# Kernel tuning notes

Hardware: AMD Instinct MI355X
Metric: run time of the kernel (lower is better)

Reference implementation:

```python
import jax, jax.numpy as jnp
import numpy as np

B, N, C, H, V = 32, 1024, 512, 256, 50  # batch, positions, post_conv_out_channels, hidden_size, out_channels


def setup_inputs() -> dict:
    key = jax.random.key(0)
    ks = jax.random.split(key, 9)
    s = 0.05
    p = lambda k, shape: jax.random.normal(k, shape, jnp.float32) * s
    return dict(
        features=jax.random.normal(ks[0], (B, N, C), jnp.float32),
        w_i2h=p(ks[1], (H, C)),              # input_to_hidden (no bias)
        w_h2h=p(ks[2], (H, H)), b_h2h=jnp.zeros((H,), jnp.float32),
        w_score=p(ks[3], (H,)),              # score Linear(H,1,no bias)
        w_gru_ih=p(ks[4], (3 * H, C + V)), w_gru_hh=p(ks[5], (3 * H, H)),
        b_gru_ih=jnp.zeros((3 * H,), jnp.float32), b_gru_hh=jnp.zeros((3 * H,), jnp.float32),
        w_s1=p(ks[6], (H, H)), b_s1=jnp.zeros((H,), jnp.float32),
        w_s2=p(ks[7], (V, H)), b_s2=jnp.zeros((V,), jnp.float32),
        max_text_length=500,
    )


def reference(features, w_i2h, w_h2h, b_h2h, w_score, w_gru_ih, w_gru_hh,
              b_gru_ih, b_gru_hh, w_s1, b_s1, w_s2, b_s2, max_text_length):
    batch = features.shape[0]
    hid = w_h2h.shape[0]
    vocab = w_s2.shape[0]
    steps = max_text_length + 1
    # input_to_hidden(features) is loop-invariant -> hoist out of the recurrence
    feat_proj = jnp.einsum('bnc,hc->bnh', features, w_i2h)

    def gru_cell(x, h):
        gi = x @ w_gru_ih.T + b_gru_ih
        gh = h @ w_gru_hh.T + b_gru_hh
        i_r, i_z, i_n = jnp.split(gi, 3, axis=-1)
        h_r, h_z, h_n = jnp.split(gh, 3, axis=-1)
        r = jax.nn.sigmoid(i_r + h_r)
        z = jax.nn.sigmoid(i_z + h_z)
        n = jnp.tanh(i_n + r * h_n)
        return (1.0 - z) * n + z * h

    def step(carry, _):
        h, pre = carry
        prev_proj = h @ w_h2h.T + b_h2h                      # [B,H]
        scores = jnp.tanh(feat_proj + prev_proj[:, None, :]) @ w_score  # [B,N]
        alpha = jax.nn.softmax(scores, axis=1)
        ctx = jnp.einsum('bn,bnc->bc', alpha, features)      # [B,C]
        onehot = jax.nn.one_hot(pre, vocab, dtype=features.dtype)
        h_new = gru_cell(jnp.concatenate([ctx, onehot], axis=-1), h)
        struct = (h_new @ w_s1.T + b_s1) @ w_s2.T + b_s2     # structure_generator, [B,V]
        pre_new = jnp.argmax(struct, axis=-1)
        return (h_new, pre_new), struct

    h0 = jnp.zeros((batch, hid), features.dtype)
    pre0 = jnp.zeros((batch,), jnp.int32)
    _, structs = jax.lax.scan(step, (h0, pre0), None, length=steps)  # [T,B,V]
    structs = jnp.transpose(structs, (1, 0, 2))                      # [B,T,V]
    return jax.nn.softmax(structs, axis=-1)
```

## Files before the change

kernel.cpp:

```cpp
#include <hip/hip_runtime.h>
#include <math.h>

#define B_ 32
#define N_ 1024
#define C_ 512
#define H_ 256
#define V_ 50
#define T_ 501
#define CV_ 562
#define G3_ 768
#define CHUNKS_ 32
#define POSB_ 32

typedef float    f32x4 __attribute__((ext_vector_type(4)));
typedef _Float16 f16x4 __attribute__((ext_vector_type(4)));
typedef _Float16 f16x8 __attribute__((ext_vector_type(8)));

__device__ __forceinline__ float fast_rcp(float x) { return __builtin_amdgcn_rcpf(x); }
__device__ __forceinline__ float fast_tanh(float x) {
  float e = __expf(2.0f * x);
  return 1.0f - 2.0f * fast_rcp(e + 1.0f);
}
__device__ __forceinline__ float fast_sigmoid(float x) {
  return fast_rcp(1.0f + __expf(-x));
}

__global__ __launch_bounds__(256) void fp_gemm(const float* __restrict__ A,
                                               const float* __restrict__ W,
                                               _Float16* __restrict__ FPh) {
  __shared__ __align__(16) float As[16][68];
  __shared__ __align__(16) float Ws[16][68];
  const int t = threadIdx.x;
  const int m0 = blockIdx.x * 64;
  const int h0 = blockIdx.y * 64;
  const int lr = t & 63;
  const int kg = t >> 6;
  const int tx = t & 15, ty = t >> 4;
  float acc[4][4] = {};
  for (int k0 = 0; k0 < C_; k0 += 16) {
    float4 av = *(const float4*)&A[(size_t)(m0 + lr) * C_ + k0 + kg * 4];
    float4 wv = *(const float4*)&W[(size_t)(h0 + lr) * C_ + k0 + kg * 4];
    As[kg*4+0][lr] = av.x; As[kg*4+1][lr] = av.y; As[kg*4+2][lr] = av.z; As[kg*4+3][lr] = av.w;
    Ws[kg*4+0][lr] = wv.x; Ws[kg*4+1][lr] = wv.y; Ws[kg*4+2][lr] = wv.z; Ws[kg*4+3][lr] = wv.w;
    __syncthreads();
#pragma unroll
    for (int kk = 0; kk < 16; ++kk) {
      float4 a = *(const float4*)&As[kk][ty * 4];
      float4 w = *(const float4*)&Ws[kk][tx * 4];
      acc[0][0] += a.x*w.x; acc[0][1] += a.x*w.y; acc[0][2] += a.x*w.z; acc[0][3] += a.x*w.w;
      acc[1][0] += a.y*w.x; acc[1][1] += a.y*w.y; acc[1][2] += a.y*w.z; acc[1][3] += a.y*w.w;
      acc[2][0] += a.z*w.x; acc[2][1] += a.z*w.y; acc[2][2] += a.z*w.z; acc[2][3] += a.z*w.w;
      acc[3][0] += a.w*w.x; acc[3][1] += a.w*w.y; acc[3][2] += a.w*w.z; acc[3][3] += a.w*w.w;
    }
    __syncthreads();
  }
#pragma unroll
  for (int i = 0; i < 4; ++i) {
    f16x4 o;
    o.x = (_Float16)acc[i][0]; o.y = (_Float16)acc[i][1];
    o.z = (_Float16)acc[i][2]; o.w = (_Float16)acc[i][3];
    *(f16x4*)&FPh[(size_t)(m0 + ty*4 + i) * H_ + h0 + tx*4] = o;
  }
}

__global__ void feat_to_fp16(const float* __restrict__ src, _Float16* __restrict__ dst,
                             int total4) {
  int i = blockIdx.x * 256 + threadIdx.x;
  if (i >= total4) return;
  f32x4 v = *(const f32x4*)&src[(size_t)i * 4];
  f16x4 o; o.x = (_Float16)v.x; o.y = (_Float16)v.y; o.z = (_Float16)v.z; o.w = (_Float16)v.w;
  *(f16x4*)&dst[(size_t)i * 4] = o;
}

__global__ void transpose_split(const float* __restrict__ src, float* __restrict__ dstA,
                                float* __restrict__ dstB, int rows, int cols, int splitc) {
  int i = blockIdx.x * 256 + threadIdx.x;
  if (i >= rows * cols) return;
  int j = i / cols, c = i - j * cols;
  float v = src[i];
  if (c < splitc) dstA[(size_t)c * rows + j] = v;
  else            dstB[(size_t)(c - splitc) * rows + j] = v;
}

__global__ void init_kernel(const float* __restrict__ b_h2h, float* __restrict__ h,
                            float* __restrict__ pp, int* __restrict__ pre) {
  int i = blockIdx.x * blockDim.x + threadIdx.x;
  if (i < B_ * H_) { h[i] = 0.0f; pp[i] = b_h2h[i & (H_ - 1)]; }
  if (i < B_) pre[i] = 0;
}

__global__ __launch_bounds__(256) void k1_attn(
    const _Float16* __restrict__ feath, const _Float16* __restrict__ fph,
    const float* __restrict__ w_score, const float* __restrict__ pp,
    float* __restrict__ part_ctx, float* __restrict__ part_l) {
  __shared__ __align__(16) float lds_ctx[4 * C_];
  __shared__ float lds_l[4];

  const int t = threadIdx.x;
  const int wv = t >> 6;
  const int lane = t & 63;
  const int b = blockIdx.x >> 5;
  const int chunk = blockIdx.x & (CHUNKS_ - 1);

  float4 ppr = *(const float4*)&pp[b * H_ + lane * 4];
  float4 wsr = *(const float4*)&w_score[lane * 4];
  float aA0 = 0.f, aA1 = 0.f, aA2 = 0.f, aA3 = 0.f;
  float aB0 = 0.f, aB1 = 0.f, aB2 = 0.f, aB3 = 0.f;
  float lacc = 0.f;
  const _Float16* fphb = fph + (size_t)b * N_ * H_;
  const _Float16* fbb  = feath + (size_t)b * N_ * C_;
  const int n0 = chunk * POSB_ + wv * 8;
#pragma unroll 2
  for (int i = 0; i < 8; ++i) {
    const int n = n0 + i;
    f16x4 v = __builtin_nontemporal_load((const f16x4*)&fphb[(size_t)n * H_ + lane * 4]);
    float s = fast_tanh((float)v.x + ppr.x) * wsr.x + fast_tanh((float)v.y + ppr.y) * wsr.y
            + fast_tanh((float)v.z + ppr.z) * wsr.z + fast_tanh((float)v.w + ppr.w) * wsr.w;
#pragma unroll
    for (int off = 32; off > 0; off >>= 1) s += __shfl_xor(s, off);
    float p = __expf(s);
    lacc += p;
    f16x8 f = __builtin_nontemporal_load((const f16x8*)&fbb[(size_t)n * C_ + lane * 8]);
    aA0 += p * (float)f.s0; aA1 += p * (float)f.s1; aA2 += p * (float)f.s2; aA3 += p * (float)f.s3;
    aB0 += p * (float)f.s4; aB1 += p * (float)f.s5; aB2 += p * (float)f.s6; aB3 += p * (float)f.s7;
  }
  {
    float4 o0; o0.x = aA0; o0.y = aA1; o0.z = aA2; o0.w = aA3;
    float4 o1; o1.x = aB0; o1.y = aB1; o1.z = aB2; o1.w = aB3;
    *(float4*)&lds_ctx[wv * C_ + lane * 8] = o0;
    *(float4*)&lds_ctx[wv * C_ + lane * 8 + 4] = o1;
  }
  if (lane == 0) lds_l[wv] = lacc;
  __syncthreads();
  {
    float c0 = lds_ctx[t] + lds_ctx[C_ + t] + lds_ctx[2 * C_ + t] + lds_ctx[3 * C_ + t];
    float c1 = lds_ctx[t + 256] + lds_ctx[C_ + t + 256] + lds_ctx[2 * C_ + t + 256] + lds_ctx[3 * C_ + t + 256];
    float* pc = &part_ctx[((size_t)b * CHUNKS_ + chunk) * C_];
    pc[t] = c0;
    pc[t + 256] = c1;
    if (t == 0) part_l[b * CHUNKS_ + chunk] = lds_l[0] + lds_l[1] + lds_l[2] + lds_l[3];
  }
}

__global__ __launch_bounds__(512) void kred(
    const float* __restrict__ part_ctx, const float* __restrict__ part_l,
    float* __restrict__ ctx_raw, float* __restrict__ l_total) {
  const int b = blockIdx.x;
  const int t = threadIdx.x;
  const float* src = part_ctx + (size_t)b * CHUNKS_ * C_ + t;
  float s = 0.f;
#pragma unroll 8
  for (int ch = 0; ch < CHUNKS_; ++ch) s += src[(size_t)ch * C_];
  ctx_raw[b * C_ + t] = s;
  if (t < 64) {
    float lv = (t < CHUNKS_) ? part_l[b * CHUNKS_ + t] : 0.0f;
#pragma unroll
    for (int off = 32; off > 0; off >>= 1) lv += __shfl_xor(lv, off);
    if (t == 0) l_total[b] = lv;
  }
}

__global__ __launch_bounds__(256) void k2a_gates(
    const float* __restrict__ ctx_raw, const float* __restrict__ h,
    const float* __restrict__ WtA, const float* __restrict__ WtH,
    float* __restrict__ pgi, float* __restrict__ pgh) {
  __shared__ __align__(16) float wlds[64][64];
  __shared__ __align__(16) float clds[32][64];
  const int t = threadIdx.x;
  const int j0 = blockIdx.x * 64;
  const int ks = blockIdx.y;
  const int jl = (t & 31) * 2;
  const int b0 = (t >> 5) * 4;

  float acc[2][4] = {};
#pragma unroll
  for (int kt = 0; kt < 2; ++kt) {
    const int k0 = ks * 128 + kt * 64;
    __syncthreads();
#pragma unroll
    for (int q = 0; q < 4; ++q) {
      int idx = q * 256 + t; int r = idx >> 4, f4 = (idx & 15) * 4;
      *(float4*)&wlds[r][f4] = *(const float4*)&WtA[(size_t)(k0 + r) * G3_ + j0 + f4];
    }
#pragma unroll
    for (int q = 0; q < 2; ++q) {
      int idx = q * 256 + t; int bb = idx >> 4, f4 = (idx & 15) * 4;
      *(float4*)&clds[bb][f4] = *(const float4*)&ctx_raw[(size_t)bb * C_ + k0 + f4];
    }
    __syncthreads();
#pragma unroll 8
    for (int k = 0; k < 64; ++k) {
      float w0 = wlds[k][jl], w1 = wlds[k][jl + 1];
      float x0 = clds[b0][k], x1 = clds[b0 + 1][k], x2 = clds[b0 + 2][k], x3 = clds[b0 + 3][k];
      acc[0][0] += w0 * x0; acc[0][1] += w0 * x1; acc[0][2] += w0 * x2; acc[0][3] += w0 * x3;
      acc[1][0] += w1 * x0; acc[1][1] += w1 * x1; acc[1][2] += w1 * x2; acc[1][3] += w1 * x3;
    }
  }
#pragma unroll
  for (int i = 0; i < 2; ++i)
#pragma unroll
    for (int q = 0; q < 4; ++q)
      pgi[((size_t)ks * B_ + b0 + q) * G3_ + j0 + jl + i] = acc[i][q];

  float acb[2][4] = {};
  {
    const int k0 = ks * 64;
    __syncthreads();
#pragma unroll
    for (int q = 0; q < 4; ++q) {
      int idx = q * 256 + t; int r = idx >> 4, f4 = (idx & 15) * 4;
      *(float4*)&wlds[r][f4] = *(const float4*)&WtH[(size_t)(k0 + r) * G3_ + j0 + f4];
    }
#pragma unroll
    for (int q = 0; q < 2; ++q) {
      int idx = q * 256 + t; int bb = idx >> 4, f4 = (idx & 15) * 4;
      *(float4*)&clds[bb][f4] = *(const float4*)&h[(size_t)bb * H_ + k0 + f4];
    }
    __syncthreads();
#pragma unroll 8
    for (int k = 0; k < 64; ++k) {
      float w0 = wlds[k][jl], w1 = wlds[k][jl + 1];
      float x0 = clds[b0][k], x1 = clds[b0 + 1][k], x2 = clds[b0 + 2][k], x3 = clds[b0 + 3][k];
      acb[0][0] += w0 * x0; acb[0][1] += w0 * x1; acb[0][2] += w0 * x2; acb[0][3] += w0 * x3;
      acb[1][0] += w1 * x0; acb[1][1] += w1 * x1; acb[1][2] += w1 * x2; acb[1][3] += w1 * x3;
    }
  }
#pragma unroll
  for (int i = 0; i < 2; ++i)
#pragma unroll
    for (int q = 0; q < 4; ++q)
      pgh[((size_t)ks * B_ + b0 + q) * G3_ + j0 + jl + i] = acb[i][q];
}

__global__ __launch_bounds__(512) void k2b_tail(
    int tstep,
    const float* __restrict__ pgi, const float* __restrict__ pgh,
    const float* __restrict__ l_total,
    const float* __restrict__ WtO,
    const float* __restrict__ b_gru_ih, const float* __restrict__ b_gru_hh,
    const float* __restrict__ Wt_s1, const float* __restrict__ b_s1,
    const float* __restrict__ Wt_h2h, const float* __restrict__ b_h2h,
    const float* __restrict__ w_s2, const float* __restrict__ b_s2,
    float* __restrict__ h, float* __restrict__ pp, int* __restrict__ pre,
    float* __restrict__ out) {
  __shared__ __align__(16) float shn[H_];
  __shared__ __align__(16) float ss1[H_];
  __shared__ float sst[64];
  const int b = blockIdx.x;
  const int t = threadIdx.x;
  const int prev = pre[b];
  const float invl = 1.0f / l_total[b];

  if (t < H_) {
    float gi0 = 0.f, gi1 = 0.f, gi2 = 0.f, gh0 = 0.f, gh1 = 0.f, gh2 = 0.f;
#pragma unroll
    for (int ks = 0; ks < 4; ++ks) {
      const float* pg = pgi + ((size_t)ks * B_ + b) * G3_;
      const float* ph = pgh + ((size_t)ks * B_ + b) * G3_;
      gi0 += pg[t]; gi1 += pg[t + 256]; gi2 += pg[t + 512];
      gh0 += ph[t]; gh1 += ph[t + 256]; gh2 += ph[t + 512];
    }
    const float* wo = WtO + (size_t)prev * G3_;
    gi0 = gi0 * invl + b_gru_ih[t]       + wo[t];
    gi1 = gi1 * invl + b_gru_ih[t + 256] + wo[t + 256];
    gi2 = gi2 * invl + b_gru_ih[t + 512] + wo[t + 512];
    gh0 += b_gru_hh[t]; gh1 += b_gru_hh[t + 256]; gh2 += b_gru_hh[t + 512];
    const float h_old = h[b * H_ + t];
    const float r = fast_sigmoid(gi0 + gh0);
    const float z = fast_sigmoid(gi1 + gh1);
    const float nn = fast_tanh(gi2 + r * gh2);
    const float hnew = (1.0f - z) * nn + z * h_old;
    h[b * H_ + t] = hnew;
    shn[t] = hnew;
  }
  __syncthreads();

  if (t < H_) {
    float acc = b_s1[t];
    const float* w1 = Wt_s1 + t;
#pragma unroll 8
    for (int c = 0; c < H_; ++c) acc += w1[(size_t)c * H_] * shn[c];
    ss1[t] = acc;
  } else if (t < 2 * H_) {
    const int tt = t - H_;
    float acc = b_h2h[tt];
    const float* wh2 = Wt_h2h + tt;
#pragma unroll 8
    for (int c = 0; c < H_; ++c) acc += wh2[(size_t)c * H_] * shn[c];
    pp[b * H_ + tt] = acc;
  }
  __syncthreads();

  const int wv = t >> 6, lane = t & 63;
  for (int v = wv; v < V_; v += 8) {
    float4 wr = *(const float4*)&w_s2[(size_t)v * H_ + lane * 4];
    float4 sv = *(const float4*)&ss1[lane * 4];
    float acc = wr.x * sv.x + wr.y * sv.y + wr.z * sv.z + wr.w * sv.w;
#pragma unroll
    for (int off = 32; off > 0; off >>= 1) acc += __shfl_xor(acc, off);
    if (lane == 0) sst[v] = acc + b_s2[v];
  }
  __syncthreads();

  if (t < 64) {
    float val = (lane < V_) ? sst[lane] : -INFINITY;
    float m = val;
#pragma unroll
    for (int off = 32; off > 0; off >>= 1) m = fmaxf(m, __shfl_xor(m, off));
    unsigned long long msk = __ballot(val == m);
    int amax = __ffsll(msk) - 1;
    float e = (lane < V_) ? __expf(val - m) : 0.0f;
    float ssum = e;
#pragma unroll
    for (int off = 32; off > 0; off >>= 1) ssum += __shfl_xor(ssum, off);
    if (lane < V_) out[((size_t)b * T_ + tstep) * V_ + lane] = e / ssum;
    if (lane == 0) pre[b] = amax;
  }
}

extern "C" void kernel_launch(void* const* d_in, const int* in_sizes, int n_in,
                              void* d_out, int out_size, void* d_ws, size_t ws_size,
                              hipStream_t stream) {
  (void)in_sizes; (void)n_in; (void)out_size; (void)ws_size;
  const float* feat     = (const float*)d_in[0];
  const float* w_i2h    = (const float*)d_in[1];
  const float* w_h2h    = (const float*)d_in[2];
  const float* b_h2h    = (const float*)d_in[3];
  const float* w_score  = (const float*)d_in[4];
  const float* w_gru_ih = (const float*)d_in[5];
  const float* w_gru_hh = (const float*)d_in[6];
  const float* b_gru_ih = (const float*)d_in[7];
  const float* b_gru_hh = (const float*)d_in[8];
  const float* w_s1     = (const float*)d_in[9];
  const float* b_s1     = (const float*)d_in[10];
  const float* w_s2     = (const float*)d_in[11];
  const float* b_s2     = (const float*)d_in[12];
  float* out = (float*)d_out;

  char* ws = (char*)d_ws;
  size_t off = 0;
  auto alloc = [&](size_t bytes) { void* p = ws + off; off += (bytes + 255) & ~(size_t)255; return p; };
  _Float16* fph   = (_Float16*)alloc((size_t)B_ * N_ * H_ * 2);
  _Float16* feath = (_Float16*)alloc((size_t)B_ * N_ * C_ * 2);
  float* part_ctx = (float*)alloc((size_t)B_ * CHUNKS_ * C_ * 4);
  float* part_l   = (float*)alloc((size_t)B_ * CHUNKS_ * 4);
  float* ctx_raw  = (float*)alloc((size_t)B_ * C_ * 4);
  float* l_total  = (float*)alloc((size_t)B_ * 4);
  float* pgi      = (float*)alloc((size_t)4 * B_ * G3_ * 4);
  float* pgh      = (float*)alloc((size_t)4 * B_ * G3_ * 4);
  float* WtA      = (float*)alloc((size_t)C_ * G3_ * 4);
  float* WtO      = (float*)alloc((size_t)V_ * G3_ * 4);
  float* WtH      = (float*)alloc((size_t)H_ * G3_ * 4);
  float* Wt_s1    = (float*)alloc((size_t)H_ * H_ * 4);
  float* Wt_h2h   = (float*)alloc((size_t)H_ * H_ * 4);
  float* h        = (float*)alloc((size_t)B_ * H_ * 4);
  float* pp       = (float*)alloc((size_t)B_ * H_ * 4);
  int*   pre      = (int*)alloc((size_t)B_ * 4);

  init_kernel<<<32, 256, 0, stream>>>(b_h2h, h, pp, pre);
  fp_gemm<<<dim3((B_ * N_) / 64, H_ / 64), 256, 0, stream>>>(feat, w_i2h, fph);
  feat_to_fp16<<<(B_ * N_ * C_ / 4 + 255) / 256, 256, 0, stream>>>(feat, feath, B_ * N_ * C_ / 4);
  transpose_split<<<(G3_ * CV_ + 255) / 256, 256, 0, stream>>>(w_gru_ih, WtA, WtO, G3_, CV_, C_);
  transpose_split<<<(G3_ * H_ + 255) / 256, 256, 0, stream>>>(w_gru_hh, WtH, WtH, G3_, H_, H_);
  transpose_split<<<(H_ * H_ + 255) / 256, 256, 0, stream>>>(w_s1, Wt_s1, Wt_s1, H_, H_, H_);
  transpose_split<<<(H_ * H_ + 255) / 256, 256, 0, stream>>>(w_h2h, Wt_h2h, Wt_h2h, H_, H_, H_);

  for (int tstep = 0; tstep < T_; ++tstep) {
    k1_attn<<<B_ * CHUNKS_, 256, 0, stream>>>(feath, fph, w_score, pp, part_ctx, part_l);
    kred<<<B_, 512, 0, stream>>>(part_ctx, part_l, ctx_raw, l_total);
    k2a_gates<<<dim3(12, 4), 256, 0, stream>>>(ctx_raw, h, WtA, WtH, pgi, pgh);
    k2b_tail<<<B_, 512, 0, stream>>>(tstep, pgi, pgh, l_total, WtO,
                                     b_gru_ih, b_gru_hh, Wt_s1, b_s1, Wt_h2h, b_h2h,
                                     w_s2, b_s2, h, pp, pre, out);
  }
}
```

Measured before the change: 15.99 ms.

## Fuse per-step reduction and GRU tail into fewer kernels with atomic last-block handoff

Drops the separate reduction kernel: the last attention block per batch element, chosen by an atomic ticket counter, sums the partial contexts. The gate GEMM and GRU tail are merged into one 48-block kernel. The first 16 blocks to finish exit, and the remaining 32 spin until all 48 have published their gate partials, then each runs the GRU update and output head for one batch element. This cuts per-step kernel launches from four to two. The cost is atomic counters, relaxed atomic loads and stores, and a spin-wait that assumes all 48 blocks are co-resident.

```diff
diff --git a/kernel.cpp b/kernel.cpp
--- a/kernel.cpp
+++ b/kernel.cpp
@@ -23,6 +23,15 @@
 }
 __device__ __forceinline__ float fast_sigmoid(float x) {
   return fast_rcp(1.0f + __expf(-x));
+}
+__device__ __forceinline__ void astore(float* p, float v) {
+  __hip_atomic_store(p, v, __ATOMIC_RELAXED, __HIP_MEMORY_SCOPE_AGENT);
+}
+__device__ __forceinline__ float aload(const float* p) {
+  return __hip_atomic_load(p, __ATOMIC_RELAXED, __HIP_MEMORY_SCOPE_AGENT);
+}
+__device__ __forceinline__ int aloadi(const int* p) {
+  return __hip_atomic_load(p, __ATOMIC_RELAXED, __HIP_MEMORY_SCOPE_AGENT);
 }
 
 __global__ __launch_bounds__(256) void fp_gemm(const float* __restrict__ A,
@@ -83,18 +92,24 @@
 }
 
 __global__ void init_kernel(const float* __restrict__ b_h2h, float* __restrict__ h,
-                            float* __restrict__ pp, int* __restrict__ pre) {
+                            float* __restrict__ pp, int* __restrict__ pre,
+                            int* __restrict__ cnt1, int* __restrict__ cnt2) {
   int i = blockIdx.x * blockDim.x + threadIdx.x;
   if (i < B_ * H_) { h[i] = 0.0f; pp[i] = b_h2h[i & (H_ - 1)]; }
   if (i < B_) pre[i] = 0;
+  if (i < T_ * B_ * 16) cnt1[i] = 0;
+  if (i < T_ * 16) cnt2[i] = 0;
 }
 
 __global__ __launch_bounds__(256) void k1_attn(
+    int tstep,
     const _Float16* __restrict__ feath, const _Float16* __restrict__ fph,
     const float* __restrict__ w_score, const float* __restrict__ pp,
-    float* __restrict__ part_ctx, float* __restrict__ part_l) {
+    float* __restrict__ part_ctx, float* __restrict__ part_l, int* __restrict__ cnt1,
+    float* __restrict__ ctx_raw, float* __restrict__ l_total) {
   __shared__ __align__(16) float lds_ctx[4 * C_];
   __shared__ float lds_l[4];
+  __shared__ int sflag;
 
   const int t = threadIdx.x;
   const int wv = t >> 6;
@@ -136,169 +151,179 @@
     float c0 = lds_ctx[t] + lds_ctx[C_ + t] + lds_ctx[2 * C_ + t] + lds_ctx[3 * C_ + t];
     float c1 = lds_ctx[t + 256] + lds_ctx[C_ + t + 256] + lds_ctx[2 * C_ + t + 256] + lds_ctx[3 * C_ + t + 256];
     float* pc = &part_ctx[((size_t)b * CHUNKS_ + chunk) * C_];
-    pc[t] = c0;
-    pc[t + 256] = c1;
-    if (t == 0) part_l[b * CHUNKS_ + chunk] = lds_l[0] + lds_l[1] + lds_l[2] + lds_l[3];
-  }
-}
-
-__global__ __launch_bounds__(512) void kred(
-    const float* __restrict__ part_ctx, const float* __restrict__ part_l,
-    float* __restrict__ ctx_raw, float* __restrict__ l_total) {
-  const int b = blockIdx.x;
-  const int t = threadIdx.x;
-  const float* src = part_ctx + (size_t)b * CHUNKS_ * C_ + t;
-  float s = 0.f;
+    astore(&pc[t], c0);
+    astore(&pc[t + 256], c1);
+    if (t == 0) astore(&part_l[b * CHUNKS_ + chunk], lds_l[0] + lds_l[1] + lds_l[2] + lds_l[3]);
+  }
+  asm volatile("s_waitcnt vmcnt(0)" ::: "memory");
+  __syncthreads();
+  if (t == 0) sflag = atomicAdd(&cnt1[(tstep * B_ + b) * 16], 1);
+  __syncthreads();
+  if (sflag != CHUNKS_ - 1) return;
+
+  float d0 = 0.f, d1 = 0.f;
+  const float* src = part_ctx + (size_t)b * CHUNKS_ * C_;
 #pragma unroll 8
-  for (int ch = 0; ch < CHUNKS_; ++ch) s += src[(size_t)ch * C_];
-  ctx_raw[b * C_ + t] = s;
+  for (int ch = 0; ch < CHUNKS_; ++ch) {
+    d0 += aload(&src[(size_t)ch * C_ + t]);
+    d1 += aload(&src[(size_t)ch * C_ + t + 256]);
+  }
+  ctx_raw[b * C_ + t] = d0;
+  ctx_raw[b * C_ + t + 256] = d1;
   if (t < 64) {
-    float lv = (t < CHUNKS_) ? part_l[b * CHUNKS_ + t] : 0.0f;
+    float lv = (t < CHUNKS_) ? aload(&part_l[b * CHUNKS_ + t]) : 0.0f;
 #pragma unroll
     for (int off = 32; off > 0; off >>= 1) lv += __shfl_xor(lv, off);
     if (t == 0) l_total[b] = lv;
   }
 }
 
-__global__ __launch_bounds__(256) void k2a_gates(
-    const float* __restrict__ ctx_raw, const float* __restrict__ h,
+__global__ __launch_bounds__(256) void k2_fused(
+    int tstep,
+    const float* __restrict__ ctx_raw, float* __restrict__ h,
     const float* __restrict__ WtA, const float* __restrict__ WtH,
-    float* __restrict__ pgi, float* __restrict__ pgh) {
-  __shared__ __align__(16) float wlds[64][64];
-  __shared__ __align__(16) float clds[32][64];
-  const int t = threadIdx.x;
-  const int j0 = blockIdx.x * 64;
-  const int ks = blockIdx.y;
-  const int jl = (t & 31) * 2;
-  const int b0 = (t >> 5) * 4;
-
-  float acc[2][4] = {};
-#pragma unroll
-  for (int kt = 0; kt < 2; ++kt) {
-    const int k0 = ks * 128 + kt * 64;
-    __syncthreads();
-#pragma unroll
-    for (int q = 0; q < 4; ++q) {
-      int idx = q * 256 + t; int r = idx >> 4, f4 = (idx & 15) * 4;
-      *(float4*)&wlds[r][f4] = *(const float4*)&WtA[(size_t)(k0 + r) * G3_ + j0 + f4];
-    }
-#pragma unroll
-    for (int q = 0; q < 2; ++q) {
-      int idx = q * 256 + t; int bb = idx >> 4, f4 = (idx & 15) * 4;
-      *(float4*)&clds[bb][f4] = *(const float4*)&ctx_raw[(size_t)bb * C_ + k0 + f4];
-    }
-    __syncthreads();
-#pragma unroll 8
-    for (int k = 0; k < 64; ++k) {
-      float w0 = wlds[k][jl], w1 = wlds[k][jl + 1];
-      float x0 = clds[b0][k], x1 = clds[b0 + 1][k], x2 = clds[b0 + 2][k], x3 = clds[b0 + 3][k];
-      acc[0][0] += w0 * x0; acc[0][1] += w0 * x1; acc[0][2] += w0 * x2; acc[0][3] += w0 * x3;
-      acc[1][0] += w1 * x0; acc[1][1] += w1 * x1; acc[1][2] += w1 * x2; acc[1][3] += w1 * x3;
-    }
-  }
-#pragma unroll
-  for (int i = 0; i < 2; ++i)
-#pragma unroll
-    for (int q = 0; q < 4; ++q)
-      pgi[((size_t)ks * B_ + b0 + q) * G3_ + j0 + jl + i] = acc[i][q];
-
-  float acb[2][4] = {};
-  {
-    const int k0 = ks * 64;
-    __syncthreads();
-#pragma unroll
-    for (int q = 0; q < 4; ++q) {
-      int idx = q * 256 + t; int r = idx >> 4, f4 = (idx & 15) * 4;
-      *(float4*)&wlds[r][f4] = *(const float4*)&WtH[(size_t)(k0 + r) * G3_ + j0 + f4];
-    }
-#pragma unroll
-    for (int q = 0; q < 2; ++q) {
-      int idx = q * 256 + t; int bb = idx >> 4, f4 = (idx & 15) * 4;
-      *(float4*)&clds[bb][f4] = *(const float4*)&h[(size_t)bb * H_ + k0 + f4];
-    }
-    __syncthreads();
-#pragma unroll 8
-    for (int k = 0; k < 64; ++k) {
-      float w0 = wlds[k][jl], w1 = wlds[k][jl + 1];
-      float x0 = clds[b0][k], x1 = clds[b0 + 1][k], x2 = clds[b0 + 2][k], x3 = clds[b0 + 3][k];
-      acb[0][0] += w0 * x0; acb[0][1] += w0 * x1; acb[0][2] += w0 * x2; acb[0][3] += w0 * x3;
-      acb[1][0] += w1 * x0; acb[1][1] += w1 * x1; acb[1][2] += w1 * x2; acb[1][3] += w1 * x3;
-    }
-  }
-#pragma unroll
-  for (int i = 0; i < 2; ++i)
-#pragma unroll
-    for (int q = 0; q < 4; ++q)
-      pgh[((size_t)ks * B_ + b0 + q) * G3_ + j0 + jl + i] = acb[i][q];
-}
-
-__global__ __launch_bounds__(512) void k2b_tail(
-    int tstep,
-    const float* __restrict__ pgi, const float* __restrict__ pgh,
+    float* __restrict__ pgi, float* __restrict__ pgh,
     const float* __restrict__ l_total,
     const float* __restrict__ WtO,
     const float* __restrict__ b_gru_ih, const float* __restrict__ b_gru_hh,
     const float* __restrict__ Wt_s1, const float* __restrict__ b_s1,
     const float* __restrict__ Wt_h2h, const float* __restrict__ b_h2h,
     const float* __restrict__ w_s2, const float* __restrict__ b_s2,
-    float* __restrict__ h, float* __restrict__ pp, int* __restrict__ pre,
-    float* __restrict__ out) {
-  __shared__ __align__(16) float shn[H_];
-  __shared__ __align__(16) float ss1[H_];
-  __shared__ float sst[64];
-  const int b = blockIdx.x;
+    float* __restrict__ pp, int* __restrict__ pre,
+    int* __restrict__ cnt2, float* __restrict__ out) {
+  __shared__ __align__(16) float smem[6144];
+  __shared__ int sflag;
   const int t = threadIdx.x;
+  const int j0 = (blockIdx.x % 12) * 64;
+  const int ks = blockIdx.x / 12;
+  float* wlds = smem;
+  float* clds = smem + 4096;
+  const int jl = (t & 31) * 2;
+  const int b0 = (t >> 5) * 4;
+
+  float acc[2][4] = {};
+#pragma unroll
+  for (int kt = 0; kt < 2; ++kt) {
+    const int k0 = ks * 128 + kt * 64;
+    __syncthreads();
+#pragma unroll
+    for (int q = 0; q < 4; ++q) {
+      int idx = q * 256 + t; int r = idx >> 4, f4 = (idx & 15) * 4;
+      *(float4*)&wlds[r * 64 + f4] = *(const float4*)&WtA[(size_t)(k0 + r) * G3_ + j0 + f4];
+    }
+#pragma unroll
+    for (int q = 0; q < 2; ++q) {
+      int idx = q * 256 + t; int bb = idx >> 4, f4 = (idx & 15) * 4;
+      *(float4*)&clds[bb * 64 + f4] = *(const float4*)&ctx_raw[(size_t)bb * C_ + k0 + f4];
+    }
+    __syncthreads();
+#pragma unroll 8
+    for (int k = 0; k < 64; ++k) {
+      float w0 = wlds[k * 64 + jl], w1 = wlds[k * 64 + jl + 1];
+      float x0 = clds[b0 * 64 + k], x1 = clds[(b0 + 1) * 64 + k];
+      float x2 = clds[(b0 + 2) * 64 + k], x3 = clds[(b0 + 3) * 64 + k];
+      acc[0][0] += w0 * x0; acc[0][1] += w0 * x1; acc[0][2] += w0 * x2; acc[0][3] += w0 * x3;
+      acc[1][0] += w1 * x0; acc[1][1] += w1 * x1; acc[1][2] += w1 * x2; acc[1][3] += w1 * x3;
+    }
+  }
+#pragma unroll
+  for (int i = 0; i < 2; ++i)
+#pragma unroll
+    for (int q = 0; q < 4; ++q)
+      astore(&pgi[((size_t)ks * B_ + b0 + q) * G3_ + j0 + jl + i], acc[i][q]);
+
+  float acb[2][4] = {};
+  {
+    const int k0 = ks * 64;
+    __syncthreads();
+#pragma unroll
+    for (int q = 0; q < 4; ++q) {
+      int idx = q * 256 + t; int r = idx >> 4, f4 = (idx & 15) * 4;
+      *(float4*)&wlds[r * 64 + f4] = *(const float4*)&WtH[(size_t)(k0 + r) * G3_ + j0 + f4];
+    }
+#pragma unroll
+    for (int q = 0; q < 2; ++q) {
+      int idx = q * 256 + t; int bb = idx >> 4, f4 = (idx & 15) * 4;
+      *(float4*)&clds[bb * 64 + f4] = *(const float4*)&h[(size_t)bb * H_ + k0 + f4];
+    }
+    __syncthreads();
+#pragma unroll 8
+    for (int k = 0; k < 64; ++k) {
+      float w0 = wlds[k * 64 + jl], w1 = wlds[k * 64 + jl + 1];
+      float x0 = clds[b0 * 64 + k], x1 = clds[(b0 + 1) * 64 + k];
+      float x2 = clds[(b0 + 2) * 64 + k], x3 = clds[(b0 + 3) * 64 + k];
+      acb[0][0] += w0 * x0; acb[0][1] += w0 * x1; acb[0][2] += w0 * x2; acb[0][3] += w0 * x3;
+      acb[1][0] += w1 * x0; acb[1][1] += w1 * x1; acb[1][2] += w1 * x2; acb[1][3] += w1 * x3;
+    }
+  }
+#pragma unroll
+  for (int i = 0; i < 2; ++i)
+#pragma unroll
+    for (int q = 0; q < 4; ++q)
+      astore(&pgh[((size_t)ks * B_ + b0 + q) * G3_ + j0 + jl + i], acb[i][q]);
+
+  asm volatile("s_waitcnt vmcnt(0)" ::: "memory");
+  __syncthreads();
+  if (t == 0) sflag = atomicAdd(&cnt2[tstep * 16], 1);
+  __syncthreads();
+  const int ticket = sflag;
+  if (ticket < 16) return;
+  if (t == 0) {
+    while (aloadi(&cnt2[tstep * 16]) < 48) __builtin_amdgcn_s_sleep(2);
+  }
+  __syncthreads();
+
+  const int b = ticket - 16;
+  float* shn = smem;
+  float* ss1 = smem + 256;
+  float* sst = smem + 512;
   const int prev = pre[b];
   const float invl = 1.0f / l_total[b];
-
-  if (t < H_) {
-    float gi0 = 0.f, gi1 = 0.f, gi2 = 0.f, gh0 = 0.f, gh1 = 0.f, gh2 = 0.f;
-#pragma unroll
-    for (int ks = 0; ks < 4; ++ks) {
-      const float* pg = pgi + ((size_t)ks * B_ + b) * G3_;
-      const float* ph = pgh + ((size_t)ks * B_ + b) * G3_;
-      gi0 += pg[t]; gi1 += pg[t + 256]; gi2 += pg[t + 512];
-      gh0 += ph[t]; gh1 += ph[t + 256]; gh2 += ph[t + 512];
-    }
-    const float* wo = WtO + (size_t)prev * G3_;
-    gi0 = gi0 * invl + b_gru_ih[t]       + wo[t];
-    gi1 = gi1 * invl + b_gru_ih[t + 256] + wo[t + 256];
-    gi2 = gi2 * invl + b_gru_ih[t + 512] + wo[t + 512];
-    gh0 += b_gru_hh[t]; gh1 += b_gru_hh[t + 256]; gh2 += b_gru_hh[t + 512];
-    const float h_old = h[b * H_ + t];
-    const float r = fast_sigmoid(gi0 + gh0);
-    const float z = fast_sigmoid(gi1 + gh1);
-    const float nn = fast_tanh(gi2 + r * gh2);
-    const float hnew = (1.0f - z) * nn + z * h_old;
-    h[b * H_ + t] = hnew;
-    shn[t] = hnew;
-  }
-  __syncthreads();
-
-  if (t < H_) {
-    float acc = b_s1[t];
+  float gi0 = 0.f, gi1 = 0.f, gi2 = 0.f, gh0 = 0.f, gh1 = 0.f, gh2 = 0.f;
+#pragma unroll
+  for (int k = 0; k < 4; ++k) {
+    const float* pg = pgi + ((size_t)k * B_ + b) * G3_;
+    const float* ph = pgh + ((size_t)k * B_ + b) * G3_;
+    gi0 += aload(&pg[t]); gi1 += aload(&pg[t + 256]); gi2 += aload(&pg[t + 512]);
+    gh0 += aload(&ph[t]); gh1 += aload(&ph[t + 256]); gh2 += aload(&ph[t + 512]);
+  }
+  const float* wo = WtO + (size_t)prev * G3_;
+  gi0 = gi0 * invl + b_gru_ih[t]       + wo[t];
+  gi1 = gi1 * invl + b_gru_ih[t + 256] + wo[t + 256];
+  gi2 = gi2 * invl + b_gru_ih[t + 512] + wo[t + 512];
+  gh0 += b_gru_hh[t]; gh1 += b_gru_hh[t + 256]; gh2 += b_gru_hh[t + 512];
+  const float h_old = h[b * H_ + t];
+  const float r = fast_sigmoid(gi0 + gh0);
+  const float z = fast_sigmoid(gi1 + gh1);
+  const float nn = fast_tanh(gi2 + r * gh2);
+  const float hnew = (1.0f - z) * nn + z * h_old;
+  h[b * H_ + t] = hnew;
+  shn[t] = hnew;
+  __syncthreads();
+
+  {
+    float a1 = b_s1[t], a2 = b_h2h[t];
     const float* w1 = Wt_s1 + t;
+    const float* w2 = Wt_h2h + t;
 #pragma unroll 8
-    for (int c = 0; c < H_; ++c) acc += w1[(size_t)c * H_] * shn[c];
-    ss1[t] = acc;
-  } else if (t < 2 * H_) {
-    const int tt = t - H_;
-    float acc = b_h2h[tt];
-    const float* wh2 = Wt_h2h + tt;
-#pragma unroll 8
-    for (int c = 0; c < H_; ++c) acc += wh2[(size_t)c * H_] * shn[c];
-    pp[b * H_ + tt] = acc;
+    for (int c = 0; c < H_; ++c) {
+      float v = shn[c];
+      a1 += w1[(size_t)c * H_] * v;
+      a2 += w2[(size_t)c * H_] * v;
+    }
+    ss1[t] = a1;
+    pp[b * H_ + t] = a2;
   }
   __syncthreads();
 
   const int wv = t >> 6, lane = t & 63;
-  for (int v = wv; v < V_; v += 8) {
+  for (int v = wv; v < V_; v += 4) {
     float4 wr = *(const float4*)&w_s2[(size_t)v * H_ + lane * 4];
     float4 sv = *(const float4*)&ss1[lane * 4];
-    float acc = wr.x * sv.x + wr.y * sv.y + wr.z * sv.z + wr.w * sv.w;
-#pragma unroll
-    for (int off = 32; off > 0; off >>= 1) acc += __shfl_xor(acc, off);
-    if (lane == 0) sst[v] = acc + b_s2[v];
+    float acc2 = wr.x * sv.x + wr.y * sv.y + wr.z * sv.z + wr.w * sv.w;
+#pragma unroll
+    for (int off = 32; off > 0; off >>= 1) acc2 += __shfl_xor(acc2, off);
+    if (lane == 0) sst[v] = acc2 + b_s2[v];
   }
   __syncthreads();
 
@@ -356,8 +381,10 @@
   float* h        = (float*)alloc((size_t)B_ * H_ * 4);
   float* pp       = (float*)alloc((size_t)B_ * H_ * 4);
   int*   pre      = (int*)alloc((size_t)B_ * 4);
-
-  init_kernel<<<32, 256, 0, stream>>>(b_h2h, h, pp, pre);
+  int*   cnt1     = (int*)alloc((size_t)T_ * B_ * 16 * 4);
+  int*   cnt2     = (int*)alloc((size_t)T_ * 16 * 4);
+
+  init_kernel<<<(T_ * B_ * 16 + 255) / 256, 256, 0, stream>>>(b_h2h, h, pp, pre, cnt1, cnt2);
   fp_gemm<<<dim3((B_ * N_) / 64, H_ / 64), 256, 0, stream>>>(feat, w_i2h, fph);
   feat_to_fp16<<<(B_ * N_ * C_ / 4 + 255) / 256, 256, 0, stream>>>(feat, feath, B_ * N_ * C_ / 4);
   transpose_split<<<(G3_ * CV_ + 255) / 256, 256, 0, stream>>>(w_gru_ih, WtA, WtO, G3_, CV_, C_);
@@ -366,11 +393,10 @@
   transpose_split<<<(H_ * H_ + 255) / 256, 256, 0, stream>>>(w_h2h, Wt_h2h, Wt_h2h, H_, H_, H_);
 
   for (int tstep = 0; tstep < T_; ++tstep) {
-    k1_attn<<<B_ * CHUNKS_, 256, 0, stream>>>(feath, fph, w_score, pp, part_ctx, part_l);
-    kred<<<B_, 512, 0, stream>>>(part_ctx, part_l, ctx_raw, l_total);
-    k2a_gates<<<dim3(12, 4), 256, 0, stream>>>(ctx_raw, h, WtA, WtH, pgi, pgh);
-    k2b_tail<<<B_, 512, 0, stream>>>(tstep, pgi, pgh, l_total, WtO,
-                                     b_gru_ih, b_gru_hh, Wt_s1, b_s1, Wt_h2h, b_h2h,
-                                     w_s2, b_s2, h, pp, pre, out);
-  }
-}
+    k1_attn<<<B_ * CHUNKS_, 256, 0, stream>>>(tstep, feath, fph, w_score, pp,
+                                              part_ctx, part_l, cnt1, ctx_raw, l_total);
+    k2_fused<<<48, 256, 0, stream>>>(tstep, ctx_raw, h, WtA, WtH, pgi, pgh, l_total,
+                                     WtO, b_gru_ih, b_gru_hh, Wt_s1, b_s1, Wt_h2h, b_h2h,
+                                     w_s2, b_s2, pp, pre, cnt2, out);
+  }
+}
```

Result: slower. 18.11 ms (+13.3%).
